# Performance work log

Measured on AMD Instinct MI355X. Metric: run time of the kernel, lower is better.

Reference implementation:

```python
import jax, jax.numpy as jnp
import numpy as np

N, E, IN_DIM, OUT_DIM, R = 50000, 800000, 128, 128, 8


def setup_inputs() -> dict:
    key = jax.random.key(0)
    k1, k2, k3, k4, k5 = jax.random.split(key, 5)
    x = jax.random.normal(k1, (N, IN_DIM), dtype=jnp.float32)
    edge_index = jax.random.randint(k2, (2, E), 0, N, dtype=jnp.int32)
    edge_type = jax.random.randint(k3, (E,), 0, R, dtype=jnp.int32)
    # Xavier-uniform-ish init for parameters
    lim_w = float(np.sqrt(6.0 / (IN_DIM + OUT_DIM)))
    weight = jax.random.uniform(k4, (R, IN_DIM, OUT_DIM), dtype=jnp.float32, minval=-lim_w, maxval=lim_w)
    self_weight = jax.random.uniform(k5, (IN_DIM, OUT_DIM), dtype=jnp.float32, minval=-lim_w, maxval=lim_w)
    return {"x": x, "weight": weight, "self_weight": self_weight,
            "edge_index": edge_index, "edge_type": edge_type}


def reference(x, weight, self_weight, edge_index, edge_type):
    n = x.shape[0]
    r = weight.shape[0]
    d_out = weight.shape[2]
    src, dst = edge_index[0], edge_index[1]
    # undirected: symmetrize edges (directed=False)
    src_all = jnp.concatenate([src, dst])          # [2E]
    dst_all = jnp.concatenate([dst, src])          # [2E]
    et_all = jnp.concatenate([edge_type, edge_type])  # [2E]
    # transform all nodes by every relation weight once: [R, N, D_out]
    xw = jnp.einsum('ni,rio->rno', x, weight)
    # gather per-edge messages already transformed by their relation's W_r
    msg = xw[et_all, src_all]                      # [2E, D_out]
    # fused (relation, dst) segment id -> per-relation scatter-add
    seg = et_all.astype(jnp.int32) * n + dst_all
    agg = jax.ops.segment_sum(msg, seg, num_segments=r * n).reshape(r, n, d_out)
    deg = jax.ops.segment_sum(jnp.ones_like(seg, dtype=x.dtype), seg,
                              num_segments=r * n).reshape(r, n)
    deg_inv = jnp.where(deg > 0, 1.0 / jnp.maximum(deg, 1.0), jnp.zeros_like(deg))
    out = jnp.sum(agg * deg_inv[..., None], axis=0)  # [N, D_out]
    out = out + x @ self_weight                       # self-loop
    return out
```

## Files before the change

kernel.cpp:

```cpp
#include <hip/hip_runtime.h>

#define NN 50000
#define EE 800000
#define RR 8
#define DD 128
#define SS (NN*RR)
#define TE (2*EE)
#define NB 782
#define NBLK 391
#define NS (NB*NBLK)

typedef __attribute__((ext_vector_type(8))) short bf16x8;
typedef __attribute__((ext_vector_type(4))) float f32x4;

__device__ __forceinline__ unsigned short f2bf(float f){
  unsigned int u = __float_as_uint(f);
  u += 0x7fffu + ((u >> 16) & 1u);
  return (unsigned short)(u >> 16);
}
__device__ __forceinline__ float bf_lo(unsigned int w){ return __uint_as_float(w << 16); }
__device__ __forceinline__ float bf_hi(unsigned int w){ return __uint_as_float(w & 0xffff0000u); }

__device__ __forceinline__ void acc8(float* a, uint4 u){
  a[0] += bf_lo(u.x); a[1] += bf_hi(u.x);
  a[2] += bf_lo(u.y); a[3] += bf_hi(u.y);
  a[4] += bf_lo(u.z); a[5] += bf_hi(u.z);
  a[6] += bf_lo(u.w); a[7] += bf_hi(u.w);
}
__device__ __forceinline__ unsigned int pack2(float a, float b){
  return ((unsigned int)f2bf(b) << 16) | (unsigned int)f2bf(a);
}

__device__ __forceinline__ void dir_edge(const int* ei, const int* et, int j,
                                         int& s, int& d, int& t){
  if (j < EE){ s = ei[j]; d = ei[EE + j]; t = et[j]; }
  else { int jj = j - EE; s = ei[EE + jj]; d = ei[jj]; t = et[jj]; }
}

__global__ __launch_bounds__(256) void k_hist(const int* __restrict__ ei,
                                              const int* __restrict__ et,
                                              int* __restrict__ hist){
  __shared__ int h[NB];
  int tid = threadIdx.x, bid = blockIdx.x;
  for (int i = tid; i < NB; i += 256) h[i] = 0;
  __syncthreads();
  int j0 = bid*4096;
  for (int k = tid; k < 4096; k += 256){
    int j = j0 + k;
    if (j < TE){
      int s, d, t; dir_edge(ei, et, j, s, d, t);
      atomicAdd(&h[d >> 6], 1);
    }
  }
  __syncthreads();
  for (int i = tid; i < NB; i += 256) hist[i*NBLK + bid] = h[i];
}

__global__ __launch_bounds__(256) void k_scan1(int* __restrict__ hist,
                                               int* __restrict__ blksum){
  __shared__ int sd[256];
  int b = blockIdx.x, tid = threadIdx.x;
  int base = b*1024 + tid*4;
  int v0 = (base+0 < NS) ? hist[base+0] : 0;
  int v1 = (base+1 < NS) ? hist[base+1] : 0;
  int v2 = (base+2 < NS) ? hist[base+2] : 0;
  int v3 = (base+3 < NS) ? hist[base+3] : 0;
  int ts = v0+v1+v2+v3;
  sd[tid] = ts; __syncthreads();
  for (int o = 1; o < 256; o <<= 1){
    int t = (tid >= o) ? sd[tid-o] : 0;
    __syncthreads();
    sd[tid] += t;
    __syncthreads();
  }
  int ex = sd[tid] - ts;
  if (base+0 < NS) hist[base+0] = ex; ex += v0;
  if (base+1 < NS) hist[base+1] = ex; ex += v1;
  if (base+2 < NS) hist[base+2] = ex; ex += v2;
  if (base+3 < NS) hist[base+3] = ex;
  if (tid == 255) blksum[b] = sd[255];
}

__global__ __launch_bounds__(512) void k_scan2(int* __restrict__ blksum, int nb){
  __shared__ int sd[512];
  int tid = threadIdx.x;
  int v = (tid < nb) ? blksum[tid] : 0;
  sd[tid] = v; __syncthreads();
  for (int o = 1; o < 512; o <<= 1){
    int t = (tid >= o) ? sd[tid-o] : 0;
    __syncthreads();
    sd[tid] += t;
    __syncthreads();
  }
  if (tid < nb) blksum[tid] = sd[tid] - v;
}

__global__ __launch_bounds__(256) void k_scan3(int* __restrict__ hist,
                                               const int* __restrict__ blksum){
  int i = blockIdx.x*blockDim.x + threadIdx.x;
  if (i < NS) hist[i] += blksum[i >> 10];
}

__global__ __launch_bounds__(256) void k_part(const int* __restrict__ ei,
                                              const int* __restrict__ et,
                                              const int* __restrict__ S,
                                              unsigned int* __restrict__ P){
  __shared__ int cur[NB];
  int tid = threadIdx.x, bid = blockIdx.x;
  for (int i = tid; i < NB; i += 256) cur[i] = S[i*NBLK + bid];
  __syncthreads();
  int j0 = bid*4096;
  for (int k = tid; k < 4096; k += 256){
    int j = j0 + k;
    if (j < TE){
      int s, d, t; dir_edge(ei, et, j, s, d, t);
      int b = d >> 6;
      int p = atomicAdd(&cur[b], 1);
      P[p] = (unsigned int)s | ((unsigned int)(d & 63) << 17)
           | ((unsigned int)t << 23);
    }
  }
}

__global__ __launch_bounds__(256) void k_build(const unsigned int* __restrict__ P,
                                               const int* __restrict__ S,
                                               int* __restrict__ esrc,
                                               int* __restrict__ offs){
  __shared__ int h[512], cu[512], sd[256];
  int tid = threadIdx.x, b = blockIdx.x;
  int pstart = S[b*NBLK];
  int pend   = (b+1 < NB) ? S[(b+1)*NBLK] : TE;
  int ne = pend - pstart;
  h[2*tid] = 0; h[2*tid+1] = 0;
  __syncthreads();
  for (int k = tid; k < ne; k += 256){
    unsigned int u = P[pstart + k];
    int lseg = (int)(((u >> 17) & 63u)*8u + (u >> 23));
    atomicAdd(&h[lseg], 1);
  }
  __syncthreads();
  int v0 = h[2*tid], v1 = h[2*tid+1];
  int ts = v0 + v1;
  sd[tid] = ts; __syncthreads();
  for (int o = 1; o < 256; o <<= 1){
    int t = (tid >= o) ? sd[tid-o] : 0;
    __syncthreads();
    sd[tid] += t;
    __syncthreads();
  }
  int ex = sd[tid] - ts;
  cu[2*tid]   = pstart + ex;
  cu[2*tid+1] = pstart + ex + v0;
  int seg0 = b*512;
  if (seg0 + 2*tid     < SS) offs[seg0 + 2*tid]     = cu[2*tid];
  if (seg0 + 2*tid + 1 < SS) offs[seg0 + 2*tid + 1] = cu[2*tid+1];
  if (b == NB-1 && tid == 0) offs[SS] = TE;
  __syncthreads();
  for (int k = tid; k < ne; k += 256){
    unsigned int u = P[pstart + k];
    int lseg = (int)(((u >> 17) & 63u)*8u + (u >> 23));
    int r = atomicAdd(&cu[lseg], 1);
    esrc[r] = (int)(u & 0x1ffffu);
  }
}

__global__ __launch_bounds__(256) void k_conv(const float* __restrict__ x,
                                              const float* __restrict__ w,
                                              const float* __restrict__ sw,
                                              unsigned short* __restrict__ xb,
                                              unsigned short* __restrict__ wb){
  int i = blockIdx.x*blockDim.x + threadIdx.x;
  const int M1 = NN*DD/4;
  if (i < M1){
    float4 v = ((const float4*)x)[i];
    ushort4 o;
    o.x = f2bf(v.x); o.y = f2bf(v.y); o.z = f2bf(v.z); o.w = f2bf(v.w);
    ((ushort4*)xb)[i] = o;
  } else {
    int j = i - M1;
    if (j < 9*DD*DD){
      int r = j >> 14; int rem = j & 16383; int n = rem >> 7; int k = rem & 127;
      float v = (r < 8) ? w[r*16384 + k*128 + n] : sw[k*128 + n];
      wb[j] = f2bf(v);
    }
  }
}

__global__ __launch_bounds__(256) void k_fused(
    const unsigned short* __restrict__ xb,
    const unsigned short* __restrict__ wb,
    const int* __restrict__ offs,
    const int* __restrict__ esrc,
    float* __restrict__ out)
{
  __shared__ __align__(16) unsigned short Alds[2][32][136];
  const int tid  = threadIdx.x;
  const int wave = tid >> 6, lane = tid & 63;
  const int l15  = lane & 15, quad = lane >> 4;
  const int g    = quad;
  const int gl   = l15;
  const int gbase = g << 4;
  const int rowbase = blockIdx.x * 32;

  f32x4 C[2][2];
  #pragma unroll
  for (int m = 0; m < 2; ++m){ C[m][0] = (f32x4)(0.f); C[m][1] = (f32x4)(0.f); }

  auto gather = [&](int rr, int b){
    int v = 0;
    if (rr < 8 && lane < 16){
      int gdj = rowbase + wave*8 + (lane >> 1);
      if (gdj < NN) v = offs[gdj*8 + rr + (lane & 1)];
    }
    #pragma unroll
    for (int p = 0; p < 2; ++p){
      int rl8  = 2*g + p;
      int rowl = wave*8 + rl8;
      int gd   = rowbase + rowl;
      uint4 u = make_uint4(0u,0u,0u,0u);
      if (rr == 8){
        if (gd < NN) u = *(const uint4*)(xb + (size_t)gd*DD + gl*8);
      } else {
        int off = __shfl(v, 2*rl8);
        int end = __shfl(v, 2*rl8 + 1);
        int cnt = (gd < NN) ? (end - off) : 0;
        float a[8] = {0.f,0.f,0.f,0.f,0.f,0.f,0.f,0.f};
        int idxv = 0;
        if (gl < cnt) idxv = esrc[off + gl];
        int cm = cnt < 16 ? cnt : 16;
        int e = 0;
        for (; e + 4 <= cm; e += 4){
          int s0 = __shfl(idxv, gbase + e + 0);
          int s1 = __shfl(idxv, gbase + e + 1);
          int s2 = __shfl(idxv, gbase + e + 2);
          int s3 = __shfl(idxv, gbase + e + 3);
          uint4 u0 = *(const uint4*)(xb + (size_t)s0*DD + gl*8);
          uint4 u1 = *(const uint4*)(xb + (size_t)s1*DD + gl*8);
          uint4 u2 = *(const uint4*)(xb + (size_t)s2*DD + gl*8);
          uint4 u3 = *(const uint4*)(xb + (size_t)s3*DD + gl*8);
          acc8(a, u0); acc8(a, u1); acc8(a, u2); acc8(a, u3);
        }
        for (; e < cm; ++e){
          int s0 = __shfl(idxv, gbase + e);
          uint4 u0 = *(const uint4*)(xb + (size_t)s0*DD + gl*8);
          acc8(a, u0);
        }
        for (int e2 = 16; e2 < cnt; ++e2){
          int s0 = esrc[off + e2];
          uint4 u0 = *(const uint4*)(xb + (size_t)s0*DD + gl*8);
          acc8(a, u0);
        }
        float sc = (cnt > 0) ? (1.0f / (float)cnt) : 0.f;
        u.x = pack2(a[0]*sc, a[1]*sc);
        u.y = pack2(a[2]*sc, a[3]*sc);
        u.z = pack2(a[4]*sc, a[5]*sc);
        u.w = pack2(a[6]*sc, a[7]*sc);
      }
      *(uint4*)&Alds[b][rowl][gl*8] = u;
    }
  };

  gather(0, 0);
  __syncthreads();

  #pragma unroll 1
  for (int rr = 0; rr < 9; ++rr){
    int b = rr & 1;
    if (rr < 8) gather(rr + 1, b ^ 1);

    const unsigned short* wr = wb + rr * 16384;
    bf16x8 bfrag[2][4];
    #pragma unroll
    for (int nt = 0; nt < 2; ++nt)
      #pragma unroll
      for (int ks = 0; ks < 4; ++ks)
        bfrag[nt][ks] = *(const bf16x8*)(wr + (wave*32 + nt*16 + l15)*128 + ks*32 + quad*8);

    #pragma unroll
    for (int m = 0; m < 2; ++m){
      #pragma unroll
      for (int ks = 0; ks < 4; ++ks){
        bf16x8 af = *(const bf16x8*)&Alds[b][m*16 + l15][ks*32 + quad*8];
        C[m][0] = __builtin_amdgcn_mfma_f32_16x16x32_bf16(af, bfrag[0][ks], C[m][0], 0, 0, 0);
        C[m][1] = __builtin_amdgcn_mfma_f32_16x16x32_bf16(af, bfrag[1][ks], C[m][1], 0, 0, 0);
      }
    }
    __syncthreads();
  }

  #pragma unroll
  for (int m = 0; m < 2; ++m){
    #pragma unroll
    for (int nt = 0; nt < 2; ++nt){
      #pragma unroll
      for (int i = 0; i < 4; ++i){
        int row = m*16 + quad*4 + i;
        int gd  = rowbase + row;
        int col = wave*32 + nt*16 + l15;
        if (gd < NN) out[gd*DD + col] = C[m][nt][i];
      }
    }
  }
}

extern "C" void kernel_launch(void* const* d_in, const int* in_sizes, int n_in,
                              void* d_out, int out_size, void* d_ws, size_t ws_size,
                              hipStream_t stream){
  const float* x  = (const float*)d_in[0];
  const float* w  = (const float*)d_in[1];
  const float* sw = (const float*)d_in[2];
  const int*   ei = (const int*)d_in[3];
  const int*   et = (const int*)d_in[4];
  float* out = (float*)d_out;
  char* ws = (char*)d_ws;

  if (ws_size < (size_t)21100000) return;

  unsigned short* xb = (unsigned short*)(ws + 0);
  int*          hist = (int*)(ws + 0);
  int*        blksum = (int*)(ws + 1223168);
  unsigned int*    P = (unsigned int*)(ws + 1225216);
  int*          esrc = (int*)(ws + 12800000);
  int*          offs = (int*)(ws + 19200000);
  unsigned short* wb = (unsigned short*)(ws + 20800016);

  k_hist <<<NBLK, 256, 0, stream>>>(ei, et, hist);
  k_scan1<<<(NS + 1023)/1024, 256, 0, stream>>>(hist, blksum);
  k_scan2<<<1, 512, 0, stream>>>(blksum, (NS + 1023)/1024);
  k_scan3<<<(NS + 255)/256, 256, 0, stream>>>(hist, blksum);
  k_part <<<NBLK, 256, 0, stream>>>(ei, et, hist, P);
  k_build<<<NB, 256, 0, stream>>>(P, hist, esrc, offs);
  k_conv <<<(NN*DD/4 + 9*DD*DD + 255)/256, 256, 0, stream>>>(x, w, sw, xb, wb);
  k_fused<<<(NN + 31)/32, 256, 0, stream>>>(xb, wb, offs, esrc, out);
}
```

Baseline: 258.3 us.

## Transform-then-gather: precompute per-relation XW, global-atomic CSR build, fused agg

Changes the order from aggregate-then-transform to transform-then-aggregate. A new MFMA kernel computes X·W_r for all 8 relations plus the self weight into a bf16 buffer of about 115 MB. A single aggregation kernel per destination then gathers the pre-transformed rows with per-relation 1/deg scaling. The two-level bucket partition (hist/part/build) is replaced by a direct per-(dst, relation) degree count and placement using global atomics. The cost is more memory traffic for the XW buffer, and edge order within segments is now nondeterministic.

```diff
diff --git a/kernel.cpp b/kernel.cpp
--- a/kernel.cpp
+++ b/kernel.cpp
@@ -6,9 +6,7 @@
 #define DD 128
 #define SS (NN*RR)
 #define TE (2*EE)
-#define NB 782
-#define NBLK 391
-#define NS (NB*NBLK)
+#define SCB 391
 
 typedef __attribute__((ext_vector_type(8))) short bf16x8;
 typedef __attribute__((ext_vector_type(4))) float f32x4;
@@ -27,8 +25,11 @@
   a[4] += bf_lo(u.z); a[5] += bf_hi(u.z);
   a[6] += bf_lo(u.w); a[7] += bf_hi(u.w);
 }
-__device__ __forceinline__ unsigned int pack2(float a, float b){
-  return ((unsigned int)f2bf(b) << 16) | (unsigned int)f2bf(a);
+__device__ __forceinline__ void acc8s(float* a, uint4 u, float s){
+  a[0] += s*bf_lo(u.x); a[1] += s*bf_hi(u.x);
+  a[2] += s*bf_lo(u.y); a[3] += s*bf_hi(u.y);
+  a[4] += s*bf_lo(u.z); a[5] += s*bf_hi(u.z);
+  a[6] += s*bf_lo(u.w); a[7] += s*bf_hi(u.w);
 }
 
 __device__ __forceinline__ void dir_edge(const int* ei, const int* et, int j,
@@ -37,34 +38,26 @@
   else { int jj = j - EE; s = ei[EE + jj]; d = ei[jj]; t = et[jj]; }
 }
 
-__global__ __launch_bounds__(256) void k_hist(const int* __restrict__ ei,
-                                              const int* __restrict__ et,
-                                              int* __restrict__ hist){
-  __shared__ int h[NB];
-  int tid = threadIdx.x, bid = blockIdx.x;
-  for (int i = tid; i < NB; i += 256) h[i] = 0;
-  __syncthreads();
-  int j0 = bid*4096;
-  for (int k = tid; k < 4096; k += 256){
-    int j = j0 + k;
-    if (j < TE){
-      int s, d, t; dir_edge(ei, et, j, s, d, t);
-      atomicAdd(&h[d >> 6], 1);
-    }
-  }
-  __syncthreads();
-  for (int i = tid; i < NB; i += 256) hist[i*NBLK + bid] = h[i];
-}
-
-__global__ __launch_bounds__(256) void k_scan1(int* __restrict__ hist,
+
+__global__ __launch_bounds__(256) void k_deg(const int* __restrict__ ei,
+                                             const int* __restrict__ et,
+                                             int* __restrict__ deg){
+  for (int j = blockIdx.x*256 + threadIdx.x; j < TE; j += gridDim.x*256){
+    int s, d, t; dir_edge(ei, et, j, s, d, t);
+    atomicAdd(&deg[d*8 + t], 1);
+  }
+}
+
+__global__ __launch_bounds__(256) void k_scan1(const int* __restrict__ deg,
+                                               int* __restrict__ offs,
                                                int* __restrict__ blksum){
   __shared__ int sd[256];
   int b = blockIdx.x, tid = threadIdx.x;
   int base = b*1024 + tid*4;
-  int v0 = (base+0 < NS) ? hist[base+0] : 0;
-  int v1 = (base+1 < NS) ? hist[base+1] : 0;
-  int v2 = (base+2 < NS) ? hist[base+2] : 0;
-  int v3 = (base+3 < NS) ? hist[base+3] : 0;
+  int v0 = (base+0 < SS) ? deg[base+0] : 0;
+  int v1 = (base+1 < SS) ? deg[base+1] : 0;
+  int v2 = (base+2 < SS) ? deg[base+2] : 0;
+  int v3 = (base+3 < SS) ? deg[base+3] : 0;
   int ts = v0+v1+v2+v3;
   sd[tid] = ts; __syncthreads();
   for (int o = 1; o < 256; o <<= 1){
@@ -74,10 +67,10 @@
     __syncthreads();
   }
   int ex = sd[tid] - ts;
-  if (base+0 < NS) hist[base+0] = ex; ex += v0;
-  if (base+1 < NS) hist[base+1] = ex; ex += v1;
-  if (base+2 < NS) hist[base+2] = ex; ex += v2;
-  if (base+3 < NS) hist[base+3] = ex;
+  if (base+0 < SS) offs[base+0] = ex; ex += v0;
+  if (base+1 < SS) offs[base+1] = ex; ex += v1;
+  if (base+2 < SS) offs[base+2] = ex; ex += v2;
+  if (base+3 < SS) offs[base+3] = ex;
   if (tid == 255) blksum[b] = sd[255];
 }
 
@@ -95,72 +88,26 @@
   if (tid < nb) blksum[tid] = sd[tid] - v;
 }
 
-__global__ __launch_bounds__(256) void k_scan3(int* __restrict__ hist,
+__global__ __launch_bounds__(256) void k_scan3(int* __restrict__ offs,
+                                               int* __restrict__ cur,
                                                const int* __restrict__ blksum){
   int i = blockIdx.x*blockDim.x + threadIdx.x;
-  if (i < NS) hist[i] += blksum[i >> 10];
-}
-
-__global__ __launch_bounds__(256) void k_part(const int* __restrict__ ei,
-                                              const int* __restrict__ et,
-                                              const int* __restrict__ S,
-                                              unsigned int* __restrict__ P){
-  __shared__ int cur[NB];
-  int tid = threadIdx.x, bid = blockIdx.x;
-  for (int i = tid; i < NB; i += 256) cur[i] = S[i*NBLK + bid];
-  __syncthreads();
-  int j0 = bid*4096;
-  for (int k = tid; k < 4096; k += 256){
-    int j = j0 + k;
-    if (j < TE){
-      int s, d, t; dir_edge(ei, et, j, s, d, t);
-      int b = d >> 6;
-      int p = atomicAdd(&cur[b], 1);
-      P[p] = (unsigned int)s | ((unsigned int)(d & 63) << 17)
-           | ((unsigned int)t << 23);
-    }
-  }
-}
-
-__global__ __launch_bounds__(256) void k_build(const unsigned int* __restrict__ P,
-                                               const int* __restrict__ S,
-                                               int* __restrict__ esrc,
-                                               int* __restrict__ offs){
-  __shared__ int h[512], cu[512], sd[256];
-  int tid = threadIdx.x, b = blockIdx.x;
-  int pstart = S[b*NBLK];
-  int pend   = (b+1 < NB) ? S[(b+1)*NBLK] : TE;
-  int ne = pend - pstart;
-  h[2*tid] = 0; h[2*tid+1] = 0;
-  __syncthreads();
-  for (int k = tid; k < ne; k += 256){
-    unsigned int u = P[pstart + k];
-    int lseg = (int)(((u >> 17) & 63u)*8u + (u >> 23));
-    atomicAdd(&h[lseg], 1);
-  }
-  __syncthreads();
-  int v0 = h[2*tid], v1 = h[2*tid+1];
-  int ts = v0 + v1;
-  sd[tid] = ts; __syncthreads();
-  for (int o = 1; o < 256; o <<= 1){
-    int t = (tid >= o) ? sd[tid-o] : 0;
-    __syncthreads();
-    sd[tid] += t;
-    __syncthreads();
-  }
-  int ex = sd[tid] - ts;
-  cu[2*tid]   = pstart + ex;
-  cu[2*tid+1] = pstart + ex + v0;
-  int seg0 = b*512;
-  if (seg0 + 2*tid     < SS) offs[seg0 + 2*tid]     = cu[2*tid];
-  if (seg0 + 2*tid + 1 < SS) offs[seg0 + 2*tid + 1] = cu[2*tid+1];
-  if (b == NB-1 && tid == 0) offs[SS] = TE;
-  __syncthreads();
-  for (int k = tid; k < ne; k += 256){
-    unsigned int u = P[pstart + k];
-    int lseg = (int)(((u >> 17) & 63u)*8u + (u >> 23));
-    int r = atomicAdd(&cu[lseg], 1);
-    esrc[r] = (int)(u & 0x1ffffu);
+  if (i < SS){
+    int v = offs[i] + blksum[i >> 10];
+    offs[i] = v;
+    cur[i] = v;
+  }
+  if (i == 0) offs[SS] = TE;
+}
+
+__global__ __launch_bounds__(256) void k_place(const int* __restrict__ ei,
+                                               const int* __restrict__ et,
+                                               int* __restrict__ cur,
+                                               int* __restrict__ esrc){
+  for (int j = blockIdx.x*256 + threadIdx.x; j < TE; j += gridDim.x*256){
+    int s, d, t; dir_edge(ei, et, j, s, d, t);
+    int p = atomicAdd(&cur[d*8 + t], 1);
+    esrc[p] = s | (t << 17);
   }
 }
 
@@ -186,121 +133,137 @@
   }
 }
 
-__global__ __launch_bounds__(256) void k_fused(
+__global__ __launch_bounds__(256, 2) void k_xw(
     const unsigned short* __restrict__ xb,
     const unsigned short* __restrict__ wb,
+    unsigned short* __restrict__ xw)
+{
+  __shared__ __align__(16) unsigned short Bs[2][128*128];
+  const int tid  = threadIdx.x;
+  const int wave = tid >> 6, lane = tid & 63;
+  const int l15  = lane & 15, quad = lane >> 4;
+  const int row0 = blockIdx.x * 128 + wave * 32;
+
+  bf16x8 af[2][4];
+  #pragma unroll
+  for (int m = 0; m < 2; ++m){
+    int gr = row0 + m*16 + l15; if (gr >= NN) gr = NN - 1;
+    #pragma unroll
+    for (int ks = 0; ks < 4; ++ks)
+      af[m][ks] = *(const bf16x8*)(xb + (size_t)gr*DD + ks*32 + quad*8);
+  }
+
+  auto stage = [&](int r, int b){
+    #pragma unroll
+    for (int j = 0; j < 8; ++j){
+      int n = j*16 + wave*4 + (lane >> 4);
+      int c = lane & 15;
+      const unsigned short* gp = wb + r*16384 + n*128 + ((c ^ (n & 7)) << 3);
+      __builtin_amdgcn_global_load_lds(
+          (const __attribute__((address_space(1))) void*)gp,
+          (__attribute__((address_space(3))) void*)((char*)&Bs[b][0] + j*4096 + wave*1024),
+          16, 0, 0);
+    }
+  };
+
+  stage(0, 0);
+
+  #pragma unroll 1
+  for (int r = 0; r < 9; ++r){
+    __syncthreads();
+    if (r < 8) stage(r + 1, (r + 1) & 1);
+
+    f32x4 C[2][8];
+    #pragma unroll
+    for (int m = 0; m < 2; ++m)
+      #pragma unroll
+      for (int nt = 0; nt < 8; ++nt) C[m][nt] = (f32x4)(0.f);
+
+    const char* bb = (const char*)&Bs[r & 1][0];
+    #pragma unroll
+    for (int nt = 0; nt < 8; ++nt){
+      bf16x8 bf[4];
+      #pragma unroll
+      for (int ks = 0; ks < 4; ++ks)
+        bf[ks] = *(const bf16x8*)(bb + (nt*16 + l15)*256
+                                     + (((ks*4 + quad) ^ (l15 & 7)) << 4));
+      #pragma unroll
+      for (int ks = 0; ks < 4; ++ks){
+        C[0][nt] = __builtin_amdgcn_mfma_f32_16x16x32_bf16(af[0][ks], bf[ks], C[0][nt], 0, 0, 0);
+        C[1][nt] = __builtin_amdgcn_mfma_f32_16x16x32_bf16(af[1][ks], bf[ks], C[1][nt], 0, 0, 0);
+      }
+    }
+
+    unsigned short* xs = xw + (size_t)r * NN * DD;
+    #pragma unroll
+    for (int m = 0; m < 2; ++m)
+      #pragma unroll
+      for (int nt = 0; nt < 8; ++nt)
+        #pragma unroll
+        for (int i = 0; i < 4; ++i){
+          int gr = row0 + m*16 + quad*4 + i;
+          if (gr < NN) xs[(size_t)gr*DD + nt*16 + l15] = f2bf(C[m][nt][i]);
+        }
+  }
+}
+
+__global__ __launch_bounds__(256, 4) void k_agg(
+    const unsigned short* __restrict__ xw,
     const int* __restrict__ offs,
     const int* __restrict__ esrc,
     float* __restrict__ out)
 {
-  __shared__ __align__(16) unsigned short Alds[2][32][136];
-  const int tid  = threadIdx.x;
-  const int wave = tid >> 6, lane = tid & 63;
-  const int l15  = lane & 15, quad = lane >> 4;
-  const int g    = quad;
-  const int gl   = l15;
-  const int gbase = g << 4;
-  const int rowbase = blockIdx.x * 32;
-
-  f32x4 C[2][2];
+  const int tid   = threadIdx.x;
+  const int lane  = tid & 63;
+  const int gl    = lane & 15;
+  const int basel = lane & 48;
+  const int d     = blockIdx.x * 16 + (tid >> 4);
+
+  int o = 0;
+  if (gl < 9) o = offs[d*8 + gl];
+  int onx = __shfl(o, (basel + gl + 1) & 63);
+  int cnt = onx - o;
+  float scale = (gl < 8 && cnt > 0) ? 1.0f/(float)cnt : 0.0f;
+  int ebase = __shfl(o, basel);
+  int etot  = __shfl(o, basel + 8) - ebase;
+
+  float a[8] = {0.f,0.f,0.f,0.f,0.f,0.f,0.f,0.f};
+
+  int pk[8];
   #pragma unroll
-  for (int m = 0; m < 2; ++m){ C[m][0] = (f32x4)(0.f); C[m][1] = (f32x4)(0.f); }
-
-  auto gather = [&](int rr, int b){
-    int v = 0;
-    if (rr < 8 && lane < 16){
-      int gdj = rowbase + wave*8 + (lane >> 1);
-      if (gdj < NN) v = offs[gdj*8 + rr + (lane & 1)];
-    }
-    #pragma unroll
-    for (int p = 0; p < 2; ++p){
-      int rl8  = 2*g + p;
-      int rowl = wave*8 + rl8;
-      int gd   = rowbase + rowl;
-      uint4 u = make_uint4(0u,0u,0u,0u);
-      if (rr == 8){
-        if (gd < NN) u = *(const uint4*)(xb + (size_t)gd*DD + gl*8);
-      } else {
-        int off = __shfl(v, 2*rl8);
-        int end = __shfl(v, 2*rl8 + 1);
-        int cnt = (gd < NN) ? (end - off) : 0;
-        float a[8] = {0.f,0.f,0.f,0.f,0.f,0.f,0.f,0.f};
-        int idxv = 0;
-        if (gl < cnt) idxv = esrc[off + gl];
-        int cm = cnt < 16 ? cnt : 16;
-        int e = 0;
-        for (; e + 4 <= cm; e += 4){
-          int s0 = __shfl(idxv, gbase + e + 0);
-          int s1 = __shfl(idxv, gbase + e + 1);
-          int s2 = __shfl(idxv, gbase + e + 2);
-          int s3 = __shfl(idxv, gbase + e + 3);
-          uint4 u0 = *(const uint4*)(xb + (size_t)s0*DD + gl*8);
-          uint4 u1 = *(const uint4*)(xb + (size_t)s1*DD + gl*8);
-          uint4 u2 = *(const uint4*)(xb + (size_t)s2*DD + gl*8);
-          uint4 u3 = *(const uint4*)(xb + (size_t)s3*DD + gl*8);
-          acc8(a, u0); acc8(a, u1); acc8(a, u2); acc8(a, u3);
-        }
-        for (; e < cm; ++e){
-          int s0 = __shfl(idxv, gbase + e);
-          uint4 u0 = *(const uint4*)(xb + (size_t)s0*DD + gl*8);
-          acc8(a, u0);
-        }
-        for (int e2 = 16; e2 < cnt; ++e2){
-          int s0 = esrc[off + e2];
-          uint4 u0 = *(const uint4*)(xb + (size_t)s0*DD + gl*8);
-          acc8(a, u0);
-        }
-        float sc = (cnt > 0) ? (1.0f / (float)cnt) : 0.f;
-        u.x = pack2(a[0]*sc, a[1]*sc);
-        u.y = pack2(a[2]*sc, a[3]*sc);
-        u.z = pack2(a[4]*sc, a[5]*sc);
-        u.w = pack2(a[6]*sc, a[7]*sc);
+  for (int s = 0; s < 8; ++s) pk[s] = (s < etot) ? esrc[ebase + s] : 0;
+
+  for (int e = 0; e < etot; e += 8){
+    uint4 U[8]; float sc[8];
+    #pragma unroll
+    for (int s = 0; s < 8; ++s){
+      sc[s] = 0.f;
+      U[s] = make_uint4(0u,0u,0u,0u);
+      if (e + s < etot){
+        int rel = (pk[s] >> 17) & 7;
+        sc[s]   = __shfl(scale, basel + rel);
+        int src = pk[s] & 0x1ffff;
+        U[s] = *(const uint4*)(xw + ((size_t)rel*NN + src)*DD + gl*8);
       }
-      *(uint4*)&Alds[b][rowl][gl*8] = u;
-    }
-  };
-
-  gather(0, 0);
-  __syncthreads();
-
-  #pragma unroll 1
-  for (int rr = 0; rr < 9; ++rr){
-    int b = rr & 1;
-    if (rr < 8) gather(rr + 1, b ^ 1);
-
-    const unsigned short* wr = wb + rr * 16384;
-    bf16x8 bfrag[2][4];
-    #pragma unroll
-    for (int nt = 0; nt < 2; ++nt)
-      #pragma unroll
-      for (int ks = 0; ks < 4; ++ks)
-        bfrag[nt][ks] = *(const bf16x8*)(wr + (wave*32 + nt*16 + l15)*128 + ks*32 + quad*8);
-
-    #pragma unroll
-    for (int m = 0; m < 2; ++m){
-      #pragma unroll
-      for (int ks = 0; ks < 4; ++ks){
-        bf16x8 af = *(const bf16x8*)&Alds[b][m*16 + l15][ks*32 + quad*8];
-        C[m][0] = __builtin_amdgcn_mfma_f32_16x16x32_bf16(af, bfrag[0][ks], C[m][0], 0, 0, 0);
-        C[m][1] = __builtin_amdgcn_mfma_f32_16x16x32_bf16(af, bfrag[1][ks], C[m][1], 0, 0, 0);
-      }
-    }
-    __syncthreads();
-  }
-
-  #pragma unroll
-  for (int m = 0; m < 2; ++m){
-    #pragma unroll
-    for (int nt = 0; nt < 2; ++nt){
-      #pragma unroll
-      for (int i = 0; i < 4; ++i){
-        int row = m*16 + quad*4 + i;
-        int gd  = rowbase + row;
-        int col = wave*32 + nt*16 + l15;
-        if (gd < NN) out[gd*DD + col] = C[m][nt][i];
-      }
-    }
-  }
+    }
+    #pragma unroll
+    for (int s = 0; s < 8; ++s){
+      int en = e + 8 + s;
+      pk[s] = (en < etot) ? esrc[ebase + en] : 0;
+    }
+    #pragma unroll
+    for (int s = 0; s < 8; ++s) acc8s(a, U[s], sc[s]);
+  }
+
+  {
+    uint4 u = *(const uint4*)(xw + ((size_t)8*NN + d)*DD + gl*8);
+    acc8(a, u);
+  }
+
+  float4 v0; v0.x = a[0]; v0.y = a[1]; v0.z = a[2]; v0.w = a[3];
+  float4 v1; v1.x = a[4]; v1.y = a[5]; v1.z = a[6]; v1.w = a[7];
+  *(float4*)(out + (size_t)d*DD + gl*8)     = v0;
+  *(float4*)(out + (size_t)d*DD + gl*8 + 4) = v1;
 }
 
 extern "C" void kernel_launch(void* const* d_in, const int* in_sizes, int n_in,
@@ -314,22 +277,23 @@
   float* out = (float*)d_out;
   char* ws = (char*)d_ws;
 
-  if (ws_size < (size_t)21100000) return;
+  if (ws_size < (size_t)136295168) return;
 
   unsigned short* xb = (unsigned short*)(ws + 0);
-  int*          hist = (int*)(ws + 0);
-  int*        blksum = (int*)(ws + 1223168);
-  unsigned int*    P = (unsigned int*)(ws + 1225216);
+  int*           cur = (int*)(ws + 0);
+  int*        blksum = (int*)(ws + 1600000);
   int*          esrc = (int*)(ws + 12800000);
   int*          offs = (int*)(ws + 19200000);
   unsigned short* wb = (unsigned short*)(ws + 20800016);
-
-  k_hist <<<NBLK, 256, 0, stream>>>(ei, et, hist);
-  k_scan1<<<(NS + 1023)/1024, 256, 0, stream>>>(hist, blksum);
-  k_scan2<<<1, 512, 0, stream>>>(blksum, (NS + 1023)/1024);
-  k_scan3<<<(NS + 255)/256, 256, 0, stream>>>(hist, blksum);
-  k_part <<<NBLK, 256, 0, stream>>>(ei, et, hist, P);
-  k_build<<<NB, 256, 0, stream>>>(P, hist, esrc, offs);
+  unsigned short* xw = (unsigned short*)(ws + 21095168);
+
+  hipMemsetAsync(cur, 0, (size_t)SS*4, stream);
+  k_deg  <<<2048, 256, 0, stream>>>(ei, et, cur);
+  k_scan1<<<SCB, 256, 0, stream>>>(cur, offs, blksum);
+  k_scan2<<<1, 512, 0, stream>>>(blksum, SCB);
+  k_scan3<<<(SS + 255)/256, 256, 0, stream>>>(offs, cur, blksum);
+  k_place<<<2048, 256, 0, stream>>>(ei, et, cur, esrc);
   k_conv <<<(NN*DD/4 + 9*DD*DD + 255)/256, 256, 0, stream>>>(x, w, sw, xb, wb);
-  k_fused<<<(NN + 31)/32, 256, 0, stream>>>(xb, wb, offs, esrc, out);
-}
+  k_xw   <<<(NN + 127)/128, 256, 0, stream>>>(xb, wb, xw);
+  k_agg  <<<NN/16, 256, 0, stream>>>(xw, offs, esrc, out);
+}
```

After: 383.8 us. 1.49x slower.
